# Kernel tuning notes

Measured on AMD Instinct MI355X. Metric: run time of the kernel, lower is better.

Reference implementation:

```python
import jax, jax.numpy as jnp
import numpy as np

B, C, H, W = 2, 64, 512, 512
N = 4096            # matches per image
N_NEG = 5           # n_not_matching
MIN_DIST = 64.0     # min_distance_for_missmatches (input_size == feature size, no rescale)
NON_MATCH_WEIGHT = float(N_NEG)   # default: non_match_weight = n_not_matching
FEAT_THRESH_NOMATCH = 0.5 * C     # L2: feat_dist_threshold_nomatch**? -> 0.5**? ; original L2 uses thr**2*C but thr given as 0.5 -> 0.25*C? NOTE: original L2: 0.5**2*C
FEAT_THRESH_NOMATCH = 0.5 ** 2 * C
FEAT_THRESH_MATCH = 0.0 ** 2 * C


def _rejection_sample(coords, rng):
    # coords: [2, N] int (x, y). Return [N, N_NEG] partner indices j with
    # ||coords[:, i] - coords[:, j]|| > MIN_DIST (same acceptance rule as the
    # torch while-loop, done once up-front in numpy).
    pts = coords.T.astype(np.float64)  # [N, 2]
    j = rng.integers(0, N, size=(N, N_NEG))
    for _ in range(200):
        d = np.linalg.norm(pts[:, None, :] - pts[j], axis=-1)  # [N, N_NEG]
        bad = d <= MIN_DIST
        if not bad.any():
            break
        j[bad] = rng.integers(0, N, size=int(bad.sum()))
    return j


def setup_inputs() -> dict:
    key = jax.random.key(0)
    k1, k2, k3 = jax.random.split(key, 3)
    rng = np.random.default_rng(0)
    inputs_ref = jax.random.normal(k1, (B, C, H, W), dtype=jnp.float32)
    inputs_other = jax.random.normal(k2, (B, C, H, W), dtype=jnp.float32)
    weights = jax.random.uniform(k3, (B, N), dtype=jnp.float32)
    inds_ref_np = rng.integers(0, W, size=(B, 2, N))    # H == W, all in-range => valid_inds all True
    inds_other_np = rng.integers(0, W, size=(B, 2, N))
    rand_inds_np = np.stack([_rejection_sample(inds_ref_np[b], rng) for b in range(B)])  # [B, N, N_NEG]
    return {
        "inputs_ref": inputs_ref,
        "inputs_other": inputs_other,
        "weights": weights,
        "inds_ref": jnp.asarray(inds_ref_np, dtype=jnp.int32),
        "inds_other": jnp.asarray(inds_other_np, dtype=jnp.int32),
        "rand_inds": jnp.asarray(rand_inds_np, dtype=jnp.int32),
    }


def reference(inputs_ref, inputs_other, weights, inds_ref, inds_other, rand_inds):
    B_, C_, H_, W_ = inputs_ref.shape
    N_ = inds_ref.shape[2]
    K = rand_inds.shape[2]
    max_distance = jnp.sqrt(jnp.asarray(H_ * H_ + W_ * W_, jnp.float32))
    ref_flat = inputs_ref.reshape(B_, C_, H_ * W_)
    oth_flat = inputs_other.reshape(B_, C_, H_ * W_)
    # lin index exactly as torch: size(2) * y + x  (valid since H == W)
    lin_ref = H_ * inds_ref[:, 1, :] + inds_ref[:, 0, :]      # [B, N]
    lin_oth = H_ * inds_other[:, 1, :] + inds_other[:, 0, :]  # [B, N]
    fr = jnp.take_along_axis(ref_flat, jnp.broadcast_to(lin_ref[:, None, :], (B_, C_, N_)), axis=2)  # [B,C,N]
    fo = jnp.take_along_axis(oth_flat, jnp.broadcast_to(lin_oth[:, None, :], (B_, C_, N_)), axis=2)
    loss_match = jnp.maximum(jnp.sum((fr - fo) ** 2, axis=1), FEAT_THRESH_MATCH)  # [B, N]
    # ---- negatives: for match i, partner j = rand_inds[b, i, k] ----
    flat_j = rand_inds.reshape(B_, -1)                                  # [B, N*K]
    lin_oth_mm = jnp.take_along_axis(lin_oth, flat_j, axis=1)           # [B, N*K]
    fo_mm = jnp.take_along_axis(
        oth_flat, jnp.broadcast_to(lin_oth_mm[:, None, :], (B_, C_, N_ * K)), axis=2
    ).reshape(B_, C_, N_, K)
    loss_mm = jnp.minimum(jnp.sum((fr[:, :, :, None] - fo_mm) ** 2, axis=1), FEAT_THRESH_NOMATCH)  # [B,N,K]
    ci = inds_ref.astype(jnp.float32)                                   # [B, 2, N]
    cj = jnp.take_along_axis(
        ci, jnp.broadcast_to(flat_j[:, None, :], (B_, 2, N_ * K)), axis=2
    ).reshape(B_, 2, N_, K)
    d = jnp.sqrt(jnp.sum((ci[:, :, :, None] - cj) ** 2, axis=1))        # [B, N, K]
    w_mm = -NON_MATCH_WEIGHT * d / max_distance / K
    loss_b = jnp.sum(weights * loss_match, axis=1) + jnp.sum(w_mm * loss_mm, axis=(1, 2))  # [B]
    loss_b = loss_b / ((K + 1.0) * N_)   # size_average
    return jnp.sum(loss_b)
```

## Files before the change

kernel.cpp:

```cpp
#include <hip/hip_runtime.h>

#define BB 2
#define CC 64
#define HH 512
#define WW 512
#define NN 4096
#define KK 5
#define HWp (HH * WW)

__global__ void zero_out_kernel(float* out) { out[0] = 0.0f; }

__global__ __launch_bounds__(256) void gather_kernel(
    const float* __restrict__ inputs_ref,
    const float* __restrict__ inputs_other,
    const int*   __restrict__ inds_ref,
    const int*   __restrict__ inds_other,
    float*       __restrict__ Fr,
    float*       __restrict__ Fo)
{
    const int lane = threadIdx.x & 63;
    int w = (blockIdx.x * 256 + threadIdx.x) >> 6;
    const int g = w & 63;  w >>= 6;
    const int c = w & 63;  w >>= 6;
    const int b = w & 1;   w >>= 1;
    const int sel = w;

    const int i = g * 64 + lane;
    const int* ind = (sel ? inds_other : inds_ref) + b * 2 * NN;
    const int lin = HH * ind[NN + i] + ind[i];

    const float* src = (sel ? inputs_other : inputs_ref)
                       + (size_t)(b * CC + c) * HWp;
    float* dst = sel ? Fo : Fr;
    dst[(size_t)(b * NN + i) * CC + c] = src[lin];
}

__global__ __launch_bounds__(256) void loss_kernel(
    const float* __restrict__ Fr,
    const float* __restrict__ Fo,
    const float* __restrict__ weights,
    const int*   __restrict__ inds_ref,
    const int*   __restrict__ rand_inds,
    float*       __restrict__ out)
{
    const int tid  = threadIdx.x;
    const int lane = tid & 63;
    const int wave = tid >> 6;
    const int gidx = blockIdx.x * 4 + wave;
    const int b = gidx / NN;
    const int i = gidx - b * NN;

    const int* ir = inds_ref + b * 2 * NN;
    const int xr = ir[i];
    const int yr = ir[NN + i];
    const int* rj = rand_inds + (size_t)(b * NN + i) * KK;

    const float fr = Fr[(size_t)(b * NN + i) * CC + lane];
    const float fo = Fo[(size_t)(b * NN + i) * CC + lane];

    float s[1 + KK];
    float dist[KK];
    { const float d = fr - fo; s[0] = d * d; }
#pragma unroll
    for (int k = 0; k < KK; ++k) {
        const int j = rj[k];
        const float fm = Fo[(size_t)(b * NN + j) * CC + lane];
        const float t = fr - fm;
        s[1 + k] = t * t;
        const float dx = (float)(xr - ir[j]);
        const float dy = (float)(yr - ir[NN + j]);
        dist[k] = sqrtf(dx * dx + dy * dy);
    }

#pragma unroll
    for (int r = 0; r < 1 + KK; ++r) {
        float v = s[r];
#pragma unroll
        for (int off = 32; off > 0; off >>= 1)
            v += __shfl_xor(v, off, 64);
        s[r] = v;
    }

    __shared__ float part[4];
    if (lane == 0) {
        const float max_distance = 724.07734f;
        const float thr_nomatch  = 16.0f;
        float acc = weights[b * NN + i] * fmaxf(s[0], 0.0f);
#pragma unroll
        for (int k = 0; k < KK; ++k) {
            acc += (-dist[k] / max_distance) * fminf(s[1 + k], thr_nomatch);
        }
        part[wave] = acc * (1.0f / (float)((KK + 1) * NN));
    }
    __syncthreads();
    if (tid == 0) {
        float t = part[0] + part[1] + part[2] + part[3];
        atomicAdd(out, t);
    }
}

extern "C" void kernel_launch(void* const* d_in, const int* in_sizes, int n_in,
                              void* d_out, int out_size, void* d_ws, size_t ws_size,
                              hipStream_t stream) {
    const float* inputs_ref   = (const float*)d_in[0];
    const float* inputs_other = (const float*)d_in[1];
    const float* weights      = (const float*)d_in[2];
    const int*   inds_ref     = (const int*)d_in[3];
    const int*   inds_other   = (const int*)d_in[4];
    const int*   rand_inds    = (const int*)d_in[5];
    float* out = (float*)d_out;

    float* Fr = (float*)d_ws;
    float* Fo = Fr + (size_t)BB * NN * CC;

    zero_out_kernel<<<1, 1, 0, stream>>>(out);

    gather_kernel<<<4096, 256, 0, stream>>>(
        inputs_ref, inputs_other, inds_ref, inds_other, Fr, Fo);

    loss_kernel<<<2048, 256, 0, stream>>>(
        Fr, Fo, weights, inds_ref, rand_inds, out);
}
```

Before: 278.1 us.

## Gather 16 channels per thread with float4 stores; replace atomic sum with reduction kernel

The gather kernel now has each thread load 16 channels for one match and write them as four float4 stores, instead of one scalar per thread. The grid shrinks from 4096 to 256 blocks. This cuts index reloads and scattered strided writes. The atomicAdd into the output and the zero kernel are replaced by per-block partials summed in a single-block reduce kernel, which removes atomic contention but adds a launch. The gather now has fewer waves in flight to hide the latency of the random loads.

```diff
diff --git a/kernel.cpp b/kernel.cpp
--- a/kernel.cpp
+++ b/kernel.cpp
@@ -7,8 +7,6 @@
 #define NN 4096
 #define KK 5
 #define HWp (HH * WW)
-
-__global__ void zero_out_kernel(float* out) { out[0] = 0.0f; }
 
 __global__ __launch_bounds__(256) void gather_kernel(
     const float* __restrict__ inputs_ref,
@@ -20,19 +18,28 @@
 {
     const int lane = threadIdx.x & 63;
     int w = (blockIdx.x * 256 + threadIdx.x) >> 6;
-    const int g = w & 63;  w >>= 6;
-    const int c = w & 63;  w >>= 6;
-    const int b = w & 1;   w >>= 1;
-    const int sel = w;
+    const int chunk = w & 3;  w >>= 2;
+    const int g     = w & 63; w >>= 6;
+    const int b     = w & 1;  w >>= 1;
+    const int sel   = w;
 
     const int i = g * 64 + lane;
     const int* ind = (sel ? inds_other : inds_ref) + b * 2 * NN;
     const int lin = HH * ind[NN + i] + ind[i];
 
     const float* src = (sel ? inputs_other : inputs_ref)
-                       + (size_t)(b * CC + c) * HWp;
-    float* dst = sel ? Fo : Fr;
-    dst[(size_t)(b * NN + i) * CC + c] = src[lin];
+                       + (size_t)b * CC * HWp
+                       + (size_t)chunk * 16 * HWp
+                       + lin;
+    float v[16];
+#pragma unroll
+    for (int cc = 0; cc < 16; ++cc)
+        v[cc] = src[(size_t)cc * HWp];
+
+    float* dst = (sel ? Fo : Fr) + (size_t)(b * NN + i) * CC + chunk * 16;
+#pragma unroll
+    for (int q = 0; q < 4; ++q)
+        ((float4*)dst)[q] = make_float4(v[4*q], v[4*q+1], v[4*q+2], v[4*q+3]);
 }
 
 __global__ __launch_bounds__(256) void loss_kernel(
@@ -41,7 +48,7 @@
     const float* __restrict__ weights,
     const int*   __restrict__ inds_ref,
     const int*   __restrict__ rand_inds,
-    float*       __restrict__ out)
+    float*       __restrict__ partials)
 {
     const int tid  = threadIdx.x;
     const int lane = tid & 63;
@@ -93,10 +100,25 @@
         part[wave] = acc * (1.0f / (float)((KK + 1) * NN));
     }
     __syncthreads();
-    if (tid == 0) {
-        float t = part[0] + part[1] + part[2] + part[3];
-        atomicAdd(out, t);
-    }
+    if (tid == 0)
+        partials[blockIdx.x] = part[0] + part[1] + part[2] + part[3];
+}
+
+__global__ __launch_bounds__(256) void reduce_kernel(
+    const float* __restrict__ partials, int n, float* __restrict__ out)
+{
+    const int tid = threadIdx.x;
+    float v = 0.0f;
+    for (int idx = tid; idx < n; idx += 256)
+        v += partials[idx];
+#pragma unroll
+    for (int off = 32; off > 0; off >>= 1)
+        v += __shfl_xor(v, off, 64);
+    __shared__ float part[4];
+    if ((tid & 63) == 0) part[tid >> 6] = v;
+    __syncthreads();
+    if (tid == 0)
+        out[0] = part[0] + part[1] + part[2] + part[3];
 }
 
 extern "C" void kernel_launch(void* const* d_in, const int* in_sizes, int n_in,
@@ -112,12 +134,13 @@
 
     float* Fr = (float*)d_ws;
     float* Fo = Fr + (size_t)BB * NN * CC;
+    float* partials = Fo + (size_t)BB * NN * CC;
 
-    zero_out_kernel<<<1, 1, 0, stream>>>(out);
-
-    gather_kernel<<<4096, 256, 0, stream>>>(
+    gather_kernel<<<256, 256, 0, stream>>>(
         inputs_ref, inputs_other, inds_ref, inds_other, Fr, Fo);
 
     loss_kernel<<<2048, 256, 0, stream>>>(
-        Fr, Fo, weights, inds_ref, rand_inds, out);
+        Fr, Fo, weights, inds_ref, rand_inds, partials);
+
+    reduce_kernel<<<1, 256, 0, stream>>>(partials, 2048, out);
 }
```

Result: faster. 259.7 us (-6.6%).
